# Kernel tuning notes

Hardware: AMD Instinct MI355X
Metric: run time of the kernel (lower is better)

## Reference

```python
import jax, jax.numpy as jnp
import numpy as np

D = 1024
K = 256
B = 8192


def setup_inputs() -> dict:
    key = jax.random.key(0)
    kx, kw, kd, kp = jax.random.split(key, 4)
    x = jax.random.normal(kx, (B, D), dtype=jnp.float32)
    # scale weights ~1/sqrt(d) so the 11-matmul chain stays numerically sane
    Ws = jax.random.normal(kw, (10, D, D), dtype=jnp.float32) / jnp.sqrt(jnp.float32(D))
    W_dec = jax.random.normal(kd, (D, K), dtype=jnp.float32) / jnp.sqrt(jnp.float32(K))
    perm = jax.random.randint(kp, (K,), 0, D, dtype=jnp.int64)
    return {"x": x, "Ws": Ws, "W_dec": W_dec, "perm": perm}


def reference(x, Ws, W_dec, perm):
    # torch nn.Linear(d,d,bias=False): y = x @ W.T
    # source applies fc1..fc9, then fc9 AGAIN, then fc10 (11 matmuls, 10 weights)
    order = list(range(9)) + [8, 9]
    h = x
    for i in order:
        h = h @ Ws[i].T  # [B, D]
    y = h[:, perm]        # vectorized gather, replaces per-row python loop [B, K]
    out = y @ W_dec.T     # fc_decode: [B, D]
    return out
```

## Files before the change

kernel.cpp:

```cpp
#include <hip/hip_runtime.h>
#include <stdint.h>
#include <stddef.h>

typedef __bf16 bf16;
typedef __bf16 bf16x8 __attribute__((ext_vector_type(8)));
typedef float f32x4 __attribute__((ext_vector_type(4)));

__device__ __forceinline__ void global_to_lds16(const void* g, void* l) {
  const __attribute__((address_space(1))) unsigned* gp =
      reinterpret_cast<const __attribute__((address_space(1))) unsigned*>(
          reinterpret_cast<uintptr_t>(g));
  __attribute__((address_space(3))) unsigned* lp =
      reinterpret_cast<__attribute__((address_space(3))) unsigned*>(
          reinterpret_cast<uintptr_t>(l));
  __builtin_amdgcn_global_load_lds(gp, lp, 16, 0, 0);
}

__device__ __forceinline__ void tile8x8_swizzle(int t, int& bx, int& by) {
  bx = (((t >> 3) & 1) << 2) | (t & 3);
  by = (((t >> 4) & 3) << 1) | ((t >> 2) & 1);
}

template <typename OutT>
__device__ __forceinline__ void gemm128_body(const bf16* __restrict__ A,
                                             const bf16* __restrict__ B,
                                             OutT* __restrict__ C,
                                             int bx, int by) {
  __shared__ bf16 As[2][128 * 64];
  __shared__ bf16 Bs[2][128 * 64];

  const int tid = threadIdx.x;
  const int wave = tid >> 6, lane = tid & 63;
  const int quad = lane >> 4, l16 = lane & 15;
  const int rowBase = by * 128;
  const int colBase = bx * 128;
  const int waveM = (wave >> 1) * 64, waveN = (wave & 1) * 64;

  const int sr = tid >> 2;
  const int sc = (tid & 3) * 8;
  const bf16* Ag0 = A + (size_t)(rowBase + sr) * 1024 + sc;
  const bf16* Ag1 = Ag0 + (size_t)64 * 1024;
  const bf16* Bg0 = B + (size_t)(colBase + sr) * 1024 + sc;
  const bf16* Bg1 = Bg0 + (size_t)64 * 1024;

  const int woff = wave * 1024;

  auto issue = [&](int k0, int p) {
    char* aB = (char*)As[p] + woff;
    char* bB = (char*)Bs[p] + woff;
    global_to_lds16(Ag0 + k0,      aB);
    global_to_lds16(Ag1 + k0,      aB + 4096);
    global_to_lds16(Ag0 + k0 + 32, aB + 8192);
    global_to_lds16(Ag1 + k0 + 32, aB + 12288);
    global_to_lds16(Bg0 + k0,      bB);
    global_to_lds16(Bg1 + k0,      bB + 4096);
    global_to_lds16(Bg0 + k0 + 32, bB + 8192);
    global_to_lds16(Bg1 + k0 + 32, bB + 12288);
  };

  f32x4 acc[4][4] = {};

  issue(0, 0);
  int p = 0;
#pragma unroll 1
  for (int k0 = 0; k0 < 1024; k0 += 64, p ^= 1) {
    __syncthreads();
    if (k0 + 64 < 1024) issue(k0 + 64, p ^ 1);
#pragma unroll
    for (int kk = 0; kk < 2; kk++) {
      const bf16* base = As[p] + kk * 4096;
      const bf16* baseB = Bs[p] + kk * 4096;
      bf16x8 af[4], bfr[4];
#pragma unroll
      for (int mi = 0; mi < 4; mi++)
        af[mi] = *(const bf16x8*)(base + (waveM + mi * 16 + l16) * 32 + quad * 8);
#pragma unroll
      for (int ni = 0; ni < 4; ni++)
        bfr[ni] = *(const bf16x8*)(baseB + (waveN + ni * 16 + l16) * 32 + quad * 8);
#pragma unroll
      for (int mi = 0; mi < 4; mi++)
#pragma unroll
        for (int ni = 0; ni < 4; ni++)
          acc[mi][ni] = __builtin_amdgcn_mfma_f32_16x16x32_bf16(af[mi], bfr[ni],
                                                                acc[mi][ni], 0, 0, 0);
    }
  }

  OutT* Cb = C + (size_t)(rowBase + waveM) * 1024 + colBase + waveN;
#pragma unroll
  for (int mi = 0; mi < 4; mi++)
#pragma unroll
    for (int ni = 0; ni < 4; ni++)
#pragma unroll
      for (int r = 0; r < 4; r++)
        Cb[(size_t)(mi * 16 + quad * 4 + r) * 1024 + ni * 16 + l16] =
            (OutT)acc[mi][ni][r];
}

struct PrepArgs {
  const float* cvt_src[5]; bf16* cvt_dst[5];
  const float* tr_src[6];  bf16* tr_dst[6];
  const float* Wdec; const int* praw; bf16* Gbf;
};

__global__ __launch_bounds__(256) void prep_all(PrepArgs p) {
  __shared__ alignas(16) char smem[64 * 65 * 2];
  const int b = blockIdx.x;
  const int tid = threadIdx.x;

  if (b < 2560) {
    const int m = b >> 9, blk = b & 511;
    const float* __restrict__ src = p.cvt_src[m];
    bf16* __restrict__ dst = p.cvt_dst[m];
    const int i = (blk * 256 + tid) * 8;
    float4 a = *(const float4*)(src + i);
    float4 c = *(const float4*)(src + i + 4);
    bf16x8 o;
    o[0] = (bf16)a.x; o[1] = (bf16)a.y; o[2] = (bf16)a.z; o[3] = (bf16)a.w;
    o[4] = (bf16)c.x; o[5] = (bf16)c.y; o[6] = (bf16)c.z; o[7] = (bf16)c.w;
    *(bf16x8*)(dst + i) = o;
  } else if (b < 4096) {
    const int t = b - 2560;
    const int m = t >> 8, r = t & 255;
    const float* __restrict__ src = p.tr_src[m];
    bf16* __restrict__ dst = p.tr_dst[m];
    bf16(*tile)[65] = reinterpret_cast<bf16(*)[65]>(smem);
    const int bx = (r & 15) * 64;
    const int by = (r >> 4) * 64;
    const int tx = tid & 63;
    const int ty4 = tid >> 6;
#pragma unroll
    for (int rr = 0; rr < 16; rr++) {
      int row = ty4 * 16 + rr;
      tile[row][tx] = (bf16)src[(size_t)(by + row) * 1024 + bx + tx];
    }
    __syncthreads();
#pragma unroll
    for (int rr = 0; rr < 16; rr++) {
      int row = ty4 * 16 + rr;
      dst[(size_t)(bx + row) * 1024 + by + tx] = tile[tx][row];
    }
  } else {
    const int j = b - 4096;
    float* row = (float*)smem;
    int* perm_l = (int*)(smem + 4096);
    int* nzp = (int*)(smem + 4096 + 1024);
#pragma unroll
    for (int c = 0; c < 4; c++) row[tid * 4 + c] = 0.f;
    if (tid == 0) *nzp = 0;
    __syncthreads();
    if (tid < 128 && p.praw[2 * tid + 1] != 0) atomicOr(nzp, 1);
    __syncthreads();
    const int is64 = (*nzp == 0);
    perm_l[tid] = is64 ? p.praw[2 * tid] : p.praw[tid];
    __syncthreads();
    atomicAdd(&row[perm_l[tid]], p.Wdec[(size_t)j * 256 + tid]);
    __syncthreads();
#pragma unroll
    for (int c = 0; c < 4; c++)
      p.Gbf[(size_t)j * 1024 + tid * 4 + c] = (bf16)row[tid * 4 + c];
  }
}

struct TreeArgs {
  const bf16* A[6]; const bf16* B[6]; bf16* C[6];
  int nG;
  const float* x; bf16* xbf; int ubase;
};

__global__ __launch_bounds__(256) void tree_level(TreeArgs a) {
  const int b = blockIdx.x;
  const int gBlocks = a.nG * 64;
  if (b < gBlocks) {
    const int z = b >> 6, t = b & 63;
    int bx, by;
    tile8x8_swizzle(t, bx, by);
    gemm128_body<bf16>(a.A[z], a.B[z], a.C[z], bx, by);
  } else {
    const int u0 = a.ubase + (b - gBlocks) * 8;
#pragma unroll
    for (int u = 0; u < 8; u++) {
      const int i = (u0 + u) * 2048 + (int)threadIdx.x * 8;
      float4 v0 = *(const float4*)(a.x + i);
      float4 v1 = *(const float4*)(a.x + i + 4);
      bf16x8 o;
      o[0] = (bf16)v0.x; o[1] = (bf16)v0.y; o[2] = (bf16)v0.z; o[3] = (bf16)v0.w;
      o[4] = (bf16)v1.x; o[5] = (bf16)v1.y; o[6] = (bf16)v1.z; o[7] = (bf16)v1.w;
      *(bf16x8*)(a.xbf + i) = o;
    }
  }
}

struct L3SArgs {
  const bf16* Q0; const bf16* Q1t; bf16* R;
  const bf16* xbf; const bf16* Q2; bf16* S;
};

__global__ __launch_bounds__(256) void l3s_level(L3SArgs a) {
  const int b = blockIdx.x;
  if (b < 64) {
    int bx, by;
    tile8x8_swizzle(b, bx, by);
    gemm128_body<bf16>(a.Q0, a.Q1t, a.R, bx, by);
  } else {
    const int t = b - 64;
    gemm128_body<bf16>(a.xbf, a.Q2, a.S, t >> 6, t & 63);
  }
}

__global__ __launch_bounds__(256) void final_gemm(const bf16* __restrict__ A,
                                                  const bf16* __restrict__ B,
                                                  float* __restrict__ C) {
  const int b = blockIdx.x;
  gemm128_body<float>(A, B, C, b >> 6, b & 63);
}

extern "C" void kernel_launch(void* const* d_in, const int* in_sizes, int n_in,
                              void* d_out, int out_size, void* d_ws, size_t ws_size,
                              hipStream_t stream) {
  const float* x    = (const float*)d_in[0];
  const float* Wsrc = (const float*)d_in[1];
  const float* Wdec = (const float*)d_in[2];
  const int*   praw = (const int*)d_in[3];
  float* out = (float*)d_out;

  constexpr size_t MAT  = 1024ull * 1024ull;
  constexpr size_t SLOT = 2ull * 1024 * 1024;

  char* ws = (char*)d_ws;
  bf16* Wrm[5];
  for (int i = 0; i < 5; i++) Wrm[i] = (bf16*)(ws + (size_t)i * SLOT);
  bf16* Wt[6];
  for (int i = 0; i < 6; i++) Wt[i] = (bf16*)(ws + (size_t)(5 + i) * SLOT);
  bf16* Gbf = (bf16*)(ws + 11 * SLOT);
  bf16* xbf = (bf16*)(ws + 12 * SLOT);
  bf16* P[6];
  for (int i = 0; i < 6; i++) P[i] = (bf16*)(ws + (size_t)(20 + i) * SLOT);
  bf16* Q[3];
  for (int i = 0; i < 3; i++) Q[i] = (bf16*)(ws + (size_t)(26 + i) * SLOT);
  bf16* Rb = (bf16*)(ws + 29 * SLOT);
  bf16* Sb = (bf16*)(ws + 31 * SLOT);

  PrepArgs pa;
  const int rmIdx[5] = {1, 3, 5, 7, 8};
  for (int i = 0; i < 5; i++) { pa.cvt_src[i] = Wsrc + (size_t)rmIdx[i] * MAT; pa.cvt_dst[i] = Wrm[i]; }
  const int trIdx[6] = {0, 2, 4, 6, 8, 9};
  for (int i = 0; i < 6; i++) { pa.tr_src[i] = Wsrc + (size_t)trIdx[i] * MAT; pa.tr_dst[i] = Wt[i]; }
  pa.Wdec = Wdec; pa.praw = praw; pa.Gbf = Gbf;
  prep_all<<<dim3(5120), 256, 0, stream>>>(pa);

  TreeArgs L1{};
  const bf16* l1a[6] = {Gbf, Wt[4], Wrm[3], Wt[2], Wrm[1], Wt[0]};
  const bf16* l1b[6] = {Wt[5], Wrm[4], Wt[3], Wrm[2], Wt[1], Wrm[0]};
  for (int i = 0; i < 6; i++) { L1.A[i] = l1a[i]; L1.B[i] = l1b[i]; L1.C[i] = P[i]; }
  L1.nG = 6; L1.x = x; L1.xbf = xbf; L1.ubase = 0;
  tree_level<<<dim3(384 + 256), 256, 0, stream>>>(L1);

  TreeArgs L2{};
  const bf16* l2a[3] = {P[0], P[3], P[4]};
  const bf16* l2b[3] = {P[1], P[2], P[5]};
  for (int i = 0; i < 3; i++) { L2.A[i] = l2a[i]; L2.B[i] = l2b[i]; L2.C[i] = Q[i]; }
  L2.nG = 3; L2.x = x; L2.xbf = xbf; L2.ubase = 2048;
  tree_level<<<dim3(192 + 256), 256, 0, stream>>>(L2);

  L3SArgs l3;
  l3.Q0 = Q[0]; l3.Q1t = Q[1]; l3.R = Rb;
  l3.xbf = xbf; l3.Q2 = Q[2]; l3.S = Sb;
  l3s_level<<<dim3(576), 256, 0, stream>>>(l3);

  final_gemm<<<dim3(512), 256, 0, stream>>>(Sb, Rb, out);

  (void)in_sizes; (void)n_in; (void)out_size; (void)ws_size;
}
```

Before: 201.7 us.

## Use 256x256 eight-wave tiles with swizzled LDS for the last GEMM stages

```diff
diff --git a/kernel.cpp b/kernel.cpp
--- a/kernel.cpp
+++ b/kernel.cpp
@@ -91,6 +91,140 @@
   for (int mi = 0; mi < 4; mi++)
 #pragma unroll
     for (int ni = 0; ni < 4; ni++)
+#pragma unroll
+      for (int r = 0; r < 4; r++)
+        Cb[(size_t)(mi * 16 + quad * 4 + r) * 1024 + ni * 16 + l16] =
+            (OutT)acc[mi][ni][r];
+}
+
+template <typename OutT>
+__device__ __forceinline__ void gemm128_w8(const bf16* __restrict__ A,
+                                           const bf16* __restrict__ B,
+                                           OutT* __restrict__ C,
+                                           int bx, int by,
+                                           bf16* As, bf16* Bs) {
+  const int tid = threadIdx.x;
+  const int wave = tid >> 6, lane = tid & 63;
+  const int quad = lane >> 4, l16 = lane & 15;
+  const int rowBase = by * 128, colBase = bx * 128;
+  const int waveM = (wave >> 2) * 64;
+  const int waveN = (wave & 3) * 32;
+
+  const int sr = tid >> 2;
+  const int sc = (tid & 3) * 8;
+  const bf16* Ag = A + (size_t)(rowBase + sr) * 1024 + sc;
+  const bf16* Bg = B + (size_t)(colBase + sr) * 1024 + sc;
+  const int woff = wave * 1024;
+
+  auto issue = [&](int k0, int p) {
+    char* aB = (char*)(As + p * 8192) + woff;
+    char* bB = (char*)(Bs + p * 8192) + woff;
+    global_to_lds16(Ag + k0,      aB);
+    global_to_lds16(Ag + k0 + 32, aB + 8192);
+    global_to_lds16(Bg + k0,      bB);
+    global_to_lds16(Bg + k0 + 32, bB + 8192);
+  };
+
+  f32x4 acc[4][2] = {};
+
+  issue(0, 0);
+  int p = 0;
+#pragma unroll 1
+  for (int k0 = 0; k0 < 1024; k0 += 64, p ^= 1) {
+    __syncthreads();
+    if (k0 + 64 < 1024) issue(k0 + 64, p ^ 1);
+#pragma unroll
+    for (int kk = 0; kk < 2; kk++) {
+      const bf16* base = As + p * 8192 + kk * 4096;
+      const bf16* baseB = Bs + p * 8192 + kk * 4096;
+      bf16x8 af[4], bfr[2];
+#pragma unroll
+      for (int mi = 0; mi < 4; mi++)
+        af[mi] = *(const bf16x8*)(base + (waveM + mi * 16 + l16) * 32 + quad * 8);
+#pragma unroll
+      for (int ni = 0; ni < 2; ni++)
+        bfr[ni] = *(const bf16x8*)(baseB + (waveN + ni * 16 + l16) * 32 + quad * 8);
+#pragma unroll
+      for (int mi = 0; mi < 4; mi++)
+#pragma unroll
+        for (int ni = 0; ni < 2; ni++)
+          acc[mi][ni] = __builtin_amdgcn_mfma_f32_16x16x32_bf16(af[mi], bfr[ni],
+                                                                acc[mi][ni], 0, 0, 0);
+    }
+  }
+
+  OutT* Cb = C + (size_t)(rowBase + waveM) * 1024 + colBase + waveN;
+#pragma unroll
+  for (int mi = 0; mi < 4; mi++)
+#pragma unroll
+    for (int ni = 0; ni < 2; ni++)
+#pragma unroll
+      for (int r = 0; r < 4; r++)
+        Cb[(size_t)(mi * 16 + quad * 4 + r) * 1024 + ni * 16 + l16] =
+            (OutT)acc[mi][ni][r];
+}
+
+template <typename OutT>
+__device__ __forceinline__ void gemm256_body(const bf16* __restrict__ A,
+                                             const bf16* __restrict__ B,
+                                             OutT* __restrict__ C,
+                                             int bx, int by,
+                                             bf16* As, bf16* Bs) {
+  const int tid = threadIdx.x;
+  const int wave = tid >> 6, lane = tid & 63;
+  const int quad = lane >> 4, l16 = lane & 15;
+  const int rowBase = by * 256, colBase = bx * 256;
+  const int waveM = (wave >> 1) * 64;
+  const int waveN = (wave & 1) * 128;
+
+  const int sr = tid >> 2;
+  const int sg = (tid & 3) ^ ((tid >> 3) & 3);
+  const bf16* Ag  = A + (size_t)(rowBase + sr) * 1024 + sg * 8;
+  const bf16* Ag1 = Ag + (size_t)128 * 1024;
+  const bf16* Bg  = B + (size_t)(colBase + sr) * 1024 + sg * 8;
+  const bf16* Bg1 = Bg + (size_t)128 * 1024;
+  const int woff = wave * 1024;
+
+  auto issue = [&](int k0, int p) {
+    char* aB = (char*)(As + p * 8192) + woff;
+    char* bB = (char*)(Bs + p * 8192) + woff;
+    global_to_lds16(Ag  + k0, aB);
+    global_to_lds16(Ag1 + k0, aB + 8192);
+    global_to_lds16(Bg  + k0, bB);
+    global_to_lds16(Bg1 + k0, bB + 8192);
+  };
+
+  f32x4 acc[4][8] = {};
+
+  issue(0, 0);
+  int p = 0;
+  const int gsw = (quad ^ ((l16 >> 1) & 3)) * 8;
+#pragma unroll 1
+  for (int i = 0; i < 32; ++i, p ^= 1) {
+    __syncthreads();
+    if (i + 1 < 32) issue((i + 1) * 32, p ^ 1);
+    const bf16* bA = As + p * 8192;
+    const bf16* bB = Bs + p * 8192;
+    bf16x8 af[4], bfr[8];
+#pragma unroll
+    for (int mi = 0; mi < 4; mi++)
+      af[mi] = *(const bf16x8*)(bA + (waveM + mi * 16 + l16) * 32 + gsw);
+#pragma unroll
+    for (int ni = 0; ni < 8; ni++)
+      bfr[ni] = *(const bf16x8*)(bB + (waveN + ni * 16 + l16) * 32 + gsw);
+#pragma unroll
+    for (int mi = 0; mi < 4; mi++)
+#pragma unroll
+      for (int ni = 0; ni < 8; ni++)
+        acc[mi][ni] = __builtin_amdgcn_mfma_f32_16x16x32_bf16(af[mi], bfr[ni],
+                                                              acc[mi][ni], 0, 0, 0);
+  }
+
+  OutT* Cb = C + (size_t)(rowBase + waveM) * 1024 + colBase + waveN;
+#pragma unroll
+  for (int mi = 0; mi < 4; mi++)
+#pragma unroll
+    for (int ni = 0; ni < 8; ni++)
 #pragma unroll
       for (int r = 0; r < 4; r++)
         Cb[(size_t)(mi * 16 + quad * 4 + r) * 1024 + ni * 16 + l16] =
@@ -192,27 +326,35 @@
 }
 
 struct L3SArgs {
-  const bf16* Q0; const bf16* Q1t; bf16* R;
-  const bf16* xbf; const bf16* Q2; bf16* S;
+  const bf16* Q0; const bf16* Q1t; bf16* A8;
+  const bf16* xbf; const bf16* C4; bf16* S1;
 };
 
-__global__ __launch_bounds__(256) void l3s_level(L3SArgs a) {
+__global__ __launch_bounds__(512, 2) void l3s_level(L3SArgs a) {
+  __shared__ bf16 smem[32768];
+  bf16* As = smem;
+  bf16* Bs = smem + 16384;
   const int b = blockIdx.x;
   if (b < 64) {
     int bx, by;
     tile8x8_swizzle(b, bx, by);
-    gemm128_body<bf16>(a.Q0, a.Q1t, a.R, bx, by);
+    gemm128_w8<bf16>(a.Q0, a.Q1t, a.A8, bx, by, As, Bs);
   } else {
     const int t = b - 64;
-    gemm128_body<bf16>(a.xbf, a.Q2, a.S, t >> 6, t & 63);
-  }
-}
-
-__global__ __launch_bounds__(256) void final_gemm(const bf16* __restrict__ A,
-                                                  const bf16* __restrict__ B,
-                                                  float* __restrict__ C) {
+    const int by = (t & 7) * 4 + ((t >> 3) & 3);
+    const int bx = t >> 5;
+    gemm256_body<bf16>(a.xbf, a.C4, a.S1, bx, by, As, Bs);
+  }
+}
+
+__global__ __launch_bounds__(512, 2) void final_gemm(const bf16* __restrict__ A,
+                                                     const bf16* __restrict__ B,
+                                                     float* __restrict__ C) {
+  __shared__ bf16 smem[32768];
   const int b = blockIdx.x;
-  gemm128_body<float>(A, B, C, b >> 6, b & 63);
+  const int by = (b & 7) * 4 + ((b >> 3) & 3);
+  const int bx = b >> 5;
+  gemm256_body<float>(A, B, C, bx, by, smem, smem + 16384);
 }
 
 extern "C" void kernel_launch(void* const* d_in, const int* in_sizes, int n_in,
@@ -238,8 +380,8 @@
   for (int i = 0; i < 6; i++) P[i] = (bf16*)(ws + (size_t)(20 + i) * SLOT);
   bf16* Q[3];
   for (int i = 0; i < 3; i++) Q[i] = (bf16*)(ws + (size_t)(26 + i) * SLOT);
-  bf16* Rb = (bf16*)(ws + 29 * SLOT);
-  bf16* Sb = (bf16*)(ws + 31 * SLOT);
+  bf16* A8b = (bf16*)(ws + 29 * SLOT);
+  bf16* S1b = (bf16*)(ws + 30 * SLOT);
 
   PrepArgs pa;
   const int rmIdx[5] = {1, 3, 5, 7, 8};
@@ -264,11 +406,11 @@
   tree_level<<<dim3(192 + 256), 256, 0, stream>>>(L2);
 
   L3SArgs l3;
-  l3.Q0 = Q[0]; l3.Q1t = Q[1]; l3.R = Rb;
-  l3.xbf = xbf; l3.Q2 = Q[2]; l3.S = Sb;
-  l3s_level<<<dim3(576), 256, 0, stream>>>(l3);
-
-  final_gemm<<<dim3(512), 256, 0, stream>>>(Sb, Rb, out);
+  l3.Q0 = Q[0]; l3.Q1t = Q[1]; l3.A8 = A8b;
+  l3.xbf = xbf; l3.C4 = Q[2];  l3.S1 = S1b;
+  l3s_level<<<dim3(192), 512, 0, stream>>>(l3);
+
+  final_gemm<<<dim3(128), 512, 0, stream>>>(S1b, A8b, out);
 
   (void)in_sizes; (void)n_in; (void)out_size; (void)ws_size;
 }
```

New measurement: 214.7 us. 6.5% more time.
